# Performance work log

Hardware: AMD Instinct MI355X
Metric: run time of the kernel (lower is better)

The kernel has to match this reference:

```python
import jax, jax.numpy as jnp
import numpy as np

B, C, H, W = 16, 64, 64, 64
K = 512  # n_embeddings


def setup_inputs() -> dict:
    key = jax.random.key(0)
    k1, k2 = jax.random.split(key)
    inputs = jax.random.normal(k1, (B, C, H, W), dtype=jnp.float32)
    emb_weight = jax.random.normal(k2, (K, C), dtype=jnp.float32)
    weight = jnp.ones((K,), dtype=jnp.float32)  # EMA cluster-size buffer
    return {"inputs": inputs, "emb_weight": emb_weight, "weight": weight}


def reference(inputs, emb_weight, weight):
    sg = jax.lax.stop_gradient
    # BCHW -> BHWC
    x = jnp.transpose(inputs, (0, 2, 3, 1))  # [B,H,W,C]
    flat = x.reshape(-1, x.shape[-1])        # [N,C]
    n = flat.shape[0]
    k = emb_weight.shape[0]
    # squared euclidean distances [N,K] (argmin identical to cdist argmin)
    d = (
        jnp.sum(flat * flat, axis=-1, keepdims=True)
        - 2.0 * (flat @ emb_weight.T)
        + jnp.sum(emb_weight * emb_weight, axis=-1)
    )
    indices = jnp.argmin(d, axis=1)  # [N]
    # avg_probs = mean over rows of one-hot mask == normalized histogram
    avg_probs = jnp.bincount(indices, length=k).astype(jnp.float32) / jnp.float32(n)
    perplexity = jnp.exp(-jnp.sum(avg_probs * jnp.log(avg_probs + 1e-10)))
    # straight-through quantization
    q = emb_weight[indices].reshape(x.shape)  # [B,H,W,C]
    quantized = sg(q) + x - sg(x)
    commitment_loss = jnp.mean((sg(quantized) - x) ** 2)
    active_codes = jnp.sum(weight >= 0.01)
    out = jnp.transpose(quantized, (0, 3, 1, 2))  # back to BCHW
    return out, commitment_loss, perplexity, active_codes, indices
```

## Files before the change

kernel.cpp:

```cpp
#include <hip/hip_runtime.h>

#define HW 4096
#define CHW 262144
#define OUT_ELEMS 4194304
#define FLT_BIG 3.4e38f

typedef __attribute__((ext_vector_type(8))) short  short8;
typedef __attribute__((ext_vector_type(4))) float  floatx4;
typedef __attribute__((ext_vector_type(4))) int    intx4;


__device__ __forceinline__ unsigned bf16_rne(float f) {
    unsigned u = __float_as_uint(f);
    return (u + 0x7FFFu + ((u >> 16) & 1u)) >> 16;
}

__device__ __forceinline__ void split8(const float* f, intx4* hi, intx4* lo) {
    unsigned h[4], l[4];
#pragma unroll
    for (int j = 0; j < 4; ++j) {
        const unsigned h0 = bf16_rne(f[2 * j]);
        const unsigned h1 = bf16_rne(f[2 * j + 1]);
        const float hf0 = __uint_as_float(h0 << 16);
        const float hf1 = __uint_as_float(h1 << 16);
        const unsigned l0 = bf16_rne(f[2 * j] - hf0);
        const unsigned l1 = bf16_rne(f[2 * j + 1] - hf1);
        h[j] = h0 | (h1 << 16);
        l[j] = l0 | (l1 << 16);
    }
    *hi = intx4{(int)h[0], (int)h[1], (int)h[2], (int)h[3]};
    *lo = intx4{(int)l[0], (int)l[1], (int)l[2], (int)l[3]};
}

__global__ void vq_prep(const float* __restrict__ emb,
                        unsigned short* __restrict__ pfrag,
                        float* __restrict__ enorm) {
    const int t = threadIdx.x;
    const int lane = t & 63;
    const int code = (blockIdx.x << 2) + (t >> 6);
    const int c = lane;
    const float v = emb[(code << 6) + c];
    const unsigned hb = bf16_rne(v);
    const float hf    = __uint_as_float(hb << 16);
    const unsigned lb = bf16_rne(v - hf);
    const int nc = code >> 6, grp = (code & 63) >> 4, n = code & 15;
    const int q = (c & 31) >> 3, o = c & 7;
    const int jh = c >> 5;
    const int jl = 2 + (c >> 5);
    pfrag[((((size_t)(nc*4 + jh)*4 + grp)*4 + q)*16 + n)*8 + o] = (unsigned short)hb;
    pfrag[((((size_t)(nc*4 + jl)*4 + grp)*4 + q)*16 + n)*8 + o] = (unsigned short)lb;
    float s = v * v;
#pragma unroll
    for (int off = 32; off > 0; off >>= 1) s += __shfl_xor(s, off, 64);
    if (lane == 0) enorm[code] = -0.5f * s;
}

__global__ __launch_bounds__(256)
void vq_main(const float* __restrict__ x_in, const float* __restrict__ emb,
             const unsigned short* __restrict__ pfrag,
             const float* __restrict__ enorm,
             float* __restrict__ out, float* __restrict__ idx_out,
             double* __restrict__ ws_sse) {
    __shared__ float  b1s[2][32], b2s[2][32];
    __shared__ int    i1s[2][32], i2s[2][32];
    __shared__ int    c1i[32], c2i[32], qidx[32];
    __shared__ double parts[8][32];
    __shared__ double ls_red[4];

    const int t     = threadIdx.x;
    const int lane  = t & 63;
    const int wv    = t >> 6;
    const int col   = lane & 15;
    const int quad  = lane >> 4;
    const int blk   = blockIdx.x;
    const int mrow0 = (wv >> 1) << 4;
    const int khalf = wv & 1;
    const int ncol0 = khalf << 5;
    const int half = blk & 1;
    const int bh = blk >> 1;
    const int b = bh >> 6, h = bh & 63;
    const float* xb = x_in + (size_t)b * CHW + h * 64 + (half << 5);

    short8 Xh[2], Xl[2];
#pragma unroll
    for (int u = 0; u < 2; ++u) {
        float f[8];
#pragma unroll
        for (int j = 0; j < 8; ++j) {
            const int c = (u << 5) + (quad << 3) + j;
            f[j] = xb[(size_t)c * HW + mrow0 + col];
        }
        intx4 hi, lo;
        split8(f, &hi, &lo);
        Xh[u] = __builtin_bit_cast(short8, hi);
        Xl[u] = __builtin_bit_cast(short8, lo);
    }

    float B1a = -FLT_BIG, B2a = -FLT_BIG, B1b = -FLT_BIG, B2b = -FLT_BIG;
    int   I1a = 0x3FFFFFFF, I2a = 0x3FFFFFFF, I1b = 0x3FFFFFFF, I2b = 0x3FFFFFFF;

    const char*  pf  = (const char*)pfrag + (size_t)lane * 16 + ((size_t)khalf << 11);
    const float* enp = enorm + ncol0 + (quad << 2);

#pragma unroll 2
    for (int nc = 0; nc < 8; ++nc) {
        const char* base = pf + ((size_t)nc << 14);
        const int K0 = nc << 6;
        const floatx4 e0v = *(const floatx4*)(enp + K0);
        const floatx4 e1v = *(const floatx4*)(enp + K0 + 16);
        floatx4 a0{0.f,0.f,0.f,0.f}, a1{0.f,0.f,0.f,0.f};
#define BLD(j, g) (*(const short8*)(base + ((j) << 12) + ((g) << 10)))
        {
            const short8 e0 = BLD(0, 0), e1 = BLD(0, 1);
            a0 = __builtin_amdgcn_mfma_f32_16x16x32_bf16(e0, Xh[0], a0, 0, 0, 0);
            a1 = __builtin_amdgcn_mfma_f32_16x16x32_bf16(e1, Xh[0], a1, 0, 0, 0);
            a0 = __builtin_amdgcn_mfma_f32_16x16x32_bf16(e0, Xl[0], a0, 0, 0, 0);
            a1 = __builtin_amdgcn_mfma_f32_16x16x32_bf16(e1, Xl[0], a1, 0, 0, 0);
        }
        {
            const short8 e0 = BLD(1, 0), e1 = BLD(1, 1);
            a0 = __builtin_amdgcn_mfma_f32_16x16x32_bf16(e0, Xh[1], a0, 0, 0, 0);
            a1 = __builtin_amdgcn_mfma_f32_16x16x32_bf16(e1, Xh[1], a1, 0, 0, 0);
            a0 = __builtin_amdgcn_mfma_f32_16x16x32_bf16(e0, Xl[1], a0, 0, 0, 0);
            a1 = __builtin_amdgcn_mfma_f32_16x16x32_bf16(e1, Xl[1], a1, 0, 0, 0);
        }
        {
            const short8 e0 = BLD(2, 0), e1 = BLD(2, 1);
            a0 = __builtin_amdgcn_mfma_f32_16x16x32_bf16(e0, Xh[0], a0, 0, 0, 0);
            a1 = __builtin_amdgcn_mfma_f32_16x16x32_bf16(e1, Xh[0], a1, 0, 0, 0);
        }
        {
            const short8 e0 = BLD(3, 0), e1 = BLD(3, 1);
            a0 = __builtin_amdgcn_mfma_f32_16x16x32_bf16(e0, Xh[1], a0, 0, 0, 0);
            a1 = __builtin_amdgcn_mfma_f32_16x16x32_bf16(e1, Xh[1], a1, 0, 0, 0);
        }
#undef BLD

        const int cb = K0 + ncol0 + (quad << 2);
#pragma unroll
        for (int reg = 0; reg < 4; ++reg) {
            const float da = a0[reg] + e0v[reg];
            if (da > B1a)      { B2a = B1a; I2a = I1a; B1a = da; I1a = cb + reg; }
            else if (da > B2a) { B2a = da; I2a = cb + reg; }
            const float db = a1[reg] + e1v[reg];
            if (db > B1b)      { B2b = B1b; I2b = I1b; B1b = db; I1b = cb + 16 + reg; }
            else if (db > B2b) { B2b = db; I2b = cb + 16 + reg; }
        }
    }

    float B1, B2; int I1, I2;
    if (B1b > B1a || (B1b == B1a && I1b < I1a)) {
        B1 = B1b; I1 = I1b;
        if (B1a > B2b || (B1a == B2b && I1a < I2b)) { B2 = B1a; I2 = I1a; }
        else                                        { B2 = B2b; I2 = I2b; }
    } else {
        B1 = B1a; I1 = I1a;
        if (B1b > B2a || (B1b == B2a && I1b < I2a)) { B2 = B1b; I2 = I1b; }
        else                                        { B2 = B2a; I2 = I2a; }
    }

#pragma unroll
    for (int off = 16; off <= 32; off <<= 1) {
        const float ob1 = __shfl_xor(B1, off, 64);
        const int   oi1 = __shfl_xor(I1, off, 64);
        const float ob2 = __shfl_xor(B2, off, 64);
        const int   oi2 = __shfl_xor(I2, off, 64);
        if (ob1 > B1 || (ob1 == B1 && oi1 < I1)) {
            float nb2; int ni2;
            if (B1 > ob2 || (B1 == ob2 && I1 < oi2)) { nb2 = B1; ni2 = I1; }
            else                                     { nb2 = ob2; ni2 = oi2; }
            B1 = ob1; I1 = oi1; B2 = nb2; I2 = ni2;
        } else if (ob1 > B2 || (ob1 == B2 && oi1 < I2)) {
            B2 = ob1; I2 = oi1;
        }
    }
    if (lane < 16) {
        const int row = mrow0 + lane;
        b1s[khalf][row] = B1; b2s[khalf][row] = B2;
        i1s[khalf][row] = I1; i2s[khalf][row] = I2;
    }
    __syncthreads();

    if (t < 32) {
        const int r = t;
        float b1 = b1s[0][r], b2 = b2s[0][r];
        int   i1 = i1s[0][r], i2 = i2s[0][r];
        const float c1 = b1s[1][r]; const int j1 = i1s[1][r];
        const float c2 = b2s[1][r]; const int j2 = i2s[1][r];
        if (c1 > b1 || (c1 == b1 && j1 < i1))      { b2 = b1; i2 = i1; b1 = c1; i1 = j1; }
        else if (c1 > b2 || (c1 == b2 && j1 < i2)) { b2 = c1; i2 = j1; }
        if (c2 > b2 || (c2 == b2 && j2 < i2))      { b2 = c2; i2 = j2; }
        c1i[r] = i1; c2i[r] = i2;
    }
    __syncthreads();

    {
        const int r  = t & 31;
        const int k  = t >> 5;
        const int cq = k >> 1;
        const int code = (k & 1) ? c2i[r] : c1i[r];
        const float* ep = emb + ((size_t)code << 6) + (cq << 4);
        const float* xq = xb + r;
        double d0 = 0.0, d1 = 0.0;
#pragma unroll
        for (int cc = 0; cc < 16; cc += 2) {
            const int c = (cq << 4) + cc;
            const double f0 = (double)xq[(size_t)c * HW]       - (double)ep[cc];
            const double f1 = (double)xq[(size_t)(c + 1) * HW] - (double)ep[cc + 1];
            d0 = fma(f0, f0, d0);
            d1 = fma(f1, f1, d1);
        }
        parts[k][r] = d0 + d1;
    }
    __syncthreads();
    if (t < 32) {
        const double d1 = parts[0][t] + parts[2][t] + parts[4][t] + parts[6][t];
        const double d2 = parts[1][t] + parts[3][t] + parts[5][t] + parts[7][t];
        int i1 = c1i[t];
        const int i2 = c2i[t];
        if (d2 < d1 || (d2 == d1 && i2 < i1)) i1 = i2;
        qidx[t] = i1;
        idx_out[(blk << 5) + t] = (float)i1;
    }
    __syncthreads();

    {
        const int r  = t & 31;
        const int c0 = (t >> 5) << 3;
        const float* xp = xb + r;
        float*       op = out + (size_t)b * CHW + h * 64 + (half << 5) + r;
        const float* eq = emb + ((size_t)qidx[r] << 6);
        float sse_local = 0.f;
#pragma unroll
        for (int cc = 0; cc < 8; ++cc) {
            const int c = c0 + cc;
            const float qc = eq[c];
            const float dx = qc - xp[(size_t)c * HW];
            sse_local = fmaf(dx, dx, sse_local);
            op[(size_t)c * HW] = qc;
        }
#pragma unroll
        for (int off = 32; off > 0; off >>= 1)
            sse_local += __shfl_down(sse_local, off, 64);
        if (lane == 0) ls_red[wv] = (double)sse_local;
        __syncthreads();
        if (t == 0)
            ws_sse[blk] = (ls_red[0] + ls_red[1]) + (ls_red[2] + ls_red[3]);
    }
}

__global__ void vq_hist(const float* __restrict__ idx_out,
                        unsigned* __restrict__ part) {
    __shared__ unsigned hs[512];
    const int t = threadIdx.x;
    hs[t] = 0u; hs[t + 256] = 0u;
    __syncthreads();
    const float4* ip = (const float4*)(idx_out + (blockIdx.x << 12));
#pragma unroll
    for (int i = 0; i < 4; ++i) {
        const float4 v = ip[(i << 8) + t];
        atomicAdd(&hs[(int)v.x], 1u);
        atomicAdd(&hs[(int)v.y], 1u);
        atomicAdd(&hs[(int)v.z], 1u);
        atomicAdd(&hs[(int)v.w], 1u);
    }
    __syncthreads();
    unsigned* pp = part + (blockIdx.x << 9);
    pp[t] = hs[t]; pp[t + 256] = hs[t + 256];
}

__global__ void vq_scal(const unsigned* __restrict__ part,
                        const double* __restrict__ ws_sse,
                        const float* __restrict__ weight,
                        float* __restrict__ scal) {
    __shared__ double redt[8], reds[8];
    __shared__ int    redi[8];
    const int k = threadIdx.x;
    const int lane = k & 63, wv = k >> 6;
    unsigned cnt = 0;
#pragma unroll
    for (int p = 0; p < 16; ++p) cnt += part[(p << 9) + k];
    const double pr = (double)cnt / 65536.0;
    double term = pr * log(pr + 1e-10);
    double ssep = 0.0;
#pragma unroll
    for (int j = 0; j < 4; ++j) ssep += ws_sse[k + (j << 9)];
    int act = (weight[k] >= 0.01f) ? 1 : 0;
#pragma unroll
    for (int off = 32; off > 0; off >>= 1) {
        term += __shfl_down(term, off, 64);
        ssep += __shfl_down(ssep, off, 64);
        act  += __shfl_down(act,  off, 64);
    }
    if (lane == 0) { redt[wv] = term; reds[wv] = ssep; redi[wv] = act; }
    __syncthreads();
    if (k == 0) {
        double s = 0.0, ss = 0.0; int a = 0;
#pragma unroll
        for (int i = 0; i < 8; ++i) { s += redt[i]; ss += reds[i]; a += redi[i]; }
        scal[0] = (float)(ss / 4194304.0);
        scal[1] = (float)exp(-s);
        scal[2] = (float)a;
    }
}

extern "C" void kernel_launch(void* const* d_in, const int* in_sizes, int n_in,
                              void* d_out, int out_size, void* d_ws, size_t ws_size,
                              hipStream_t stream) {
    const float* x      = (const float*)d_in[0];
    const float* emb    = (const float*)d_in[1];
    const float* weight = (const float*)d_in[2];

    float* out = (float*)d_out;
    float*          enorm  = (float*)d_ws;
    unsigned short* pfrag  = (unsigned short*)((char*)d_ws + 4096);
    double*         ws_sse = (double*)((char*)d_ws + 135168);
    unsigned*       part   = (unsigned*)((char*)d_ws + 151552);

    float* scal    = out + OUT_ELEMS;
    float* idx_out = out + OUT_ELEMS + 3;

    vq_prep<<<128, 256, 0, stream>>>(emb, pfrag, enorm);
    vq_main<<<2048, 256, 0, stream>>>(x, emb, pfrag, enorm, out, idx_out, ws_sse);
    vq_hist<<<16, 256, 0, stream>>>(idx_out, part);
    vq_scal<<<1, 512, 0, stream>>>(part, ws_sse, weight, scal);
}
```

Before: 108.6 us.

## Halve vq_main block size and fuse histogram with scalar reduction

Each vq_main block now covers 16 pixels with two waves instead of 32 pixels with four, so the grid doubles to 4096 blocks of 128 threads. The final argmin pick is computed redundantly in every thread, which drops the shared qidx array and one barrier. The two small tail kernels (histogram and scalar reduction) are merged into one single-block kernel, removing a launch and the partial-histogram buffer. In exchange, one block must now do the whole 65536-entry histogram serially, and each pixel row is split into more, smaller blocks with less reuse of the codebook fragments per block.

```diff
diff --git a/kernel.cpp b/kernel.cpp
--- a/kernel.cpp
+++ b/kernel.cpp
@@ -55,17 +55,17 @@
     if (lane == 0) enorm[code] = -0.5f * s;
 }
 
-__global__ __launch_bounds__(256)
+__global__ __launch_bounds__(128)
 void vq_main(const float* __restrict__ x_in, const float* __restrict__ emb,
              const unsigned short* __restrict__ pfrag,
              const float* __restrict__ enorm,
              float* __restrict__ out, float* __restrict__ idx_out,
              double* __restrict__ ws_sse) {
-    __shared__ float  b1s[2][32], b2s[2][32];
-    __shared__ int    i1s[2][32], i2s[2][32];
-    __shared__ int    c1i[32], c2i[32], qidx[32];
-    __shared__ double parts[8][32];
-    __shared__ double ls_red[4];
+    __shared__ float  b1s[2][16], b2s[2][16];
+    __shared__ int    i1s[2][16], i2s[2][16];
+    __shared__ int    c1i[16], c2i[16];
+    __shared__ double parts[8][17];
+    __shared__ double ls_red[2];
 
     const int t     = threadIdx.x;
     const int lane  = t & 63;
@@ -73,13 +73,12 @@
     const int col   = lane & 15;
     const int quad  = lane >> 4;
     const int blk   = blockIdx.x;
-    const int mrow0 = (wv >> 1) << 4;
-    const int khalf = wv & 1;
+    const int khalf = wv;
     const int ncol0 = khalf << 5;
-    const int half = blk & 1;
-    const int bh = blk >> 1;
+    const int wq  = blk & 3;
+    const int bh  = blk >> 2;
     const int b = bh >> 6, h = bh & 63;
-    const float* xb = x_in + (size_t)b * CHW + h * 64 + (half << 5);
+    const float* xb = x_in + (size_t)b * CHW + h * 64 + (wq << 4);
 
     short8 Xh[2], Xl[2];
 #pragma unroll
@@ -88,7 +87,7 @@
 #pragma unroll
         for (int j = 0; j < 8; ++j) {
             const int c = (u << 5) + (quad << 3) + j;
-            f[j] = xb[(size_t)c * HW + mrow0 + col];
+            f[j] = xb[(size_t)c * HW + col];
         }
         intx4 hi, lo;
         split8(f, &hi, &lo);
@@ -175,13 +174,12 @@
         }
     }
     if (lane < 16) {
-        const int row = mrow0 + lane;
-        b1s[khalf][row] = B1; b2s[khalf][row] = B2;
-        i1s[khalf][row] = I1; i2s[khalf][row] = I2;
-    }
-    __syncthreads();
-
-    if (t < 32) {
+        b1s[khalf][lane] = B1; b2s[khalf][lane] = B2;
+        i1s[khalf][lane] = I1; i2s[khalf][lane] = I2;
+    }
+    __syncthreads();
+
+    if (t < 16) {
         const int r = t;
         float b1 = b1s[0][r], b2 = b2s[0][r];
         int   i1 = i1s[0][r], i2 = i2s[0][r];
@@ -194,9 +192,9 @@
     }
     __syncthreads();
 
+    const int r = t & 15;
+    const int k = t >> 4;
     {
-        const int r  = t & 31;
-        const int k  = t >> 5;
         const int cq = k >> 1;
         const int code = (k & 1) ? c2i[r] : c1i[r];
         const float* ep = emb + ((size_t)code << 6) + (cq << 4);
@@ -213,23 +211,22 @@
         parts[k][r] = d0 + d1;
     }
     __syncthreads();
-    if (t < 32) {
-        const double d1 = parts[0][t] + parts[2][t] + parts[4][t] + parts[6][t];
-        const double d2 = parts[1][t] + parts[3][t] + parts[5][t] + parts[7][t];
-        int i1 = c1i[t];
-        const int i2 = c2i[t];
-        if (d2 < d1 || (d2 == d1 && i2 < i1)) i1 = i2;
-        qidx[t] = i1;
-        idx_out[(blk << 5) + t] = (float)i1;
-    }
-    __syncthreads();
-
+
+    int win;
     {
-        const int r  = t & 31;
-        const int c0 = (t >> 5) << 3;
+        const double d1 = parts[0][r] + parts[2][r] + parts[4][r] + parts[6][r];
+        const double d2 = parts[1][r] + parts[3][r] + parts[5][r] + parts[7][r];
+        win = c1i[r];
+        const int i2 = c2i[r];
+        if (d2 < d1 || (d2 == d1 && i2 < win)) win = i2;
+        if (t < 16) idx_out[(blk << 4) + r] = (float)win;
+    }
+
+    {
+        const int c0 = k << 3;
         const float* xp = xb + r;
-        float*       op = out + (size_t)b * CHW + h * 64 + (half << 5) + r;
-        const float* eq = emb + ((size_t)qidx[r] << 6);
+        float*       op = out + (size_t)b * CHW + h * 64 + (wq << 4) + r;
+        const float* eq = emb + ((size_t)win << 6);
         float sse_local = 0.f;
 #pragma unroll
         for (int cc = 0; cc < 8; ++cc) {
@@ -245,47 +242,38 @@
         if (lane == 0) ls_red[wv] = (double)sse_local;
         __syncthreads();
         if (t == 0)
-            ws_sse[blk] = (ls_red[0] + ls_red[1]) + (ls_red[2] + ls_red[3]);
-    }
-}
-
-__global__ void vq_hist(const float* __restrict__ idx_out,
-                        unsigned* __restrict__ part) {
+            ws_sse[blk] = ls_red[0] + ls_red[1];
+    }
+}
+
+__global__ void vq_tail(const float* __restrict__ idx_out,
+                        const double* __restrict__ ws_sse,
+                        const float* __restrict__ weight,
+                        float* __restrict__ scal) {
     __shared__ unsigned hs[512];
+    __shared__ double redt[8], reds[8];
+    __shared__ int    redi[8];
     const int t = threadIdx.x;
-    hs[t] = 0u; hs[t + 256] = 0u;
-    __syncthreads();
-    const float4* ip = (const float4*)(idx_out + (blockIdx.x << 12));
-#pragma unroll
-    for (int i = 0; i < 4; ++i) {
-        const float4 v = ip[(i << 8) + t];
+    const int lane = t & 63, wv = t >> 6;
+    hs[t] = 0u;
+    __syncthreads();
+    const float4* ip = (const float4*)idx_out;
+#pragma unroll
+    for (int i = 0; i < 32; ++i) {
+        const float4 v = ip[(i << 9) + t];
         atomicAdd(&hs[(int)v.x], 1u);
         atomicAdd(&hs[(int)v.y], 1u);
         atomicAdd(&hs[(int)v.z], 1u);
         atomicAdd(&hs[(int)v.w], 1u);
     }
     __syncthreads();
-    unsigned* pp = part + (blockIdx.x << 9);
-    pp[t] = hs[t]; pp[t + 256] = hs[t + 256];
-}
-
-__global__ void vq_scal(const unsigned* __restrict__ part,
-                        const double* __restrict__ ws_sse,
-                        const float* __restrict__ weight,
-                        float* __restrict__ scal) {
-    __shared__ double redt[8], reds[8];
-    __shared__ int    redi[8];
-    const int k = threadIdx.x;
-    const int lane = k & 63, wv = k >> 6;
-    unsigned cnt = 0;
-#pragma unroll
-    for (int p = 0; p < 16; ++p) cnt += part[(p << 9) + k];
+    const unsigned cnt = hs[t];
     const double pr = (double)cnt / 65536.0;
     double term = pr * log(pr + 1e-10);
     double ssep = 0.0;
 #pragma unroll
-    for (int j = 0; j < 4; ++j) ssep += ws_sse[k + (j << 9)];
-    int act = (weight[k] >= 0.01f) ? 1 : 0;
+    for (int j = 0; j < 8; ++j) ssep += ws_sse[t + (j << 9)];
+    int act = (weight[t] >= 0.01f) ? 1 : 0;
 #pragma unroll
     for (int off = 32; off > 0; off >>= 1) {
         term += __shfl_down(term, off, 64);
@@ -294,7 +282,7 @@
     }
     if (lane == 0) { redt[wv] = term; reds[wv] = ssep; redi[wv] = act; }
     __syncthreads();
-    if (k == 0) {
+    if (t == 0) {
         double s = 0.0, ss = 0.0; int a = 0;
 #pragma unroll
         for (int i = 0; i < 8; ++i) { s += redt[i]; ss += reds[i]; a += redi[i]; }
@@ -315,13 +303,11 @@
     float*          enorm  = (float*)d_ws;
     unsigned short* pfrag  = (unsigned short*)((char*)d_ws + 4096);
     double*         ws_sse = (double*)((char*)d_ws + 135168);
-    unsigned*       part   = (unsigned*)((char*)d_ws + 151552);
 
     float* scal    = out + OUT_ELEMS;
     float* idx_out = out + OUT_ELEMS + 3;
 
     vq_prep<<<128, 256, 0, stream>>>(emb, pfrag, enorm);
-    vq_main<<<2048, 256, 0, stream>>>(x, emb, pfrag, enorm, out, idx_out, ws_sse);
-    vq_hist<<<16, 256, 0, stream>>>(idx_out, part);
-    vq_scal<<<1, 512, 0, stream>>>(part, ws_sse, weight, scal);
-}
+    vq_main<<<4096, 128, 0, stream>>>(x, emb, pfrag, enorm, out, idx_out, ws_sse);
+    vq_tail<<<1, 512, 0, stream>>>(idx_out, ws_sse, weight, scal);
+}
```

New measurement: 122.5 us. 12.7% more time.

## Process 64 rows per block so each codebook fragment load feeds two MFMA tiles

Applied to the files above, without the earlier changes.

Each wave now handles two 16-row tiles of pixels instead of one, so every codebook fragment loaded from global memory is reused across two sets of MFMAs. Blocks cover a full 64-pixel image row, which halves the grid, halves the number of SSE partials, and merges the winner selection into the final write phase, removing one barrier. The cost is higher register pressure from doubled accumulators and X fragments, and fewer blocks available to hide latency.

```diff
diff --git a/kernel.cpp b/kernel.cpp
--- a/kernel.cpp
+++ b/kernel.cpp
@@ -61,10 +61,10 @@
              const float* __restrict__ enorm,
              float* __restrict__ out, float* __restrict__ idx_out,
              double* __restrict__ ws_sse) {
-    __shared__ float  b1s[2][32], b2s[2][32];
-    __shared__ int    i1s[2][32], i2s[2][32];
-    __shared__ int    c1i[32], c2i[32], qidx[32];
-    __shared__ double parts[8][32];
+    __shared__ float  b1s[2][64], b2s[2][64];
+    __shared__ int    i1s[2][64], i2s[2][64];
+    __shared__ int    c1i[64], c2i[64];
+    __shared__ double parts[4][65];
     __shared__ double ls_red[4];
 
     const int t     = threadIdx.x;
@@ -73,31 +73,38 @@
     const int col   = lane & 15;
     const int quad  = lane >> 4;
     const int blk   = blockIdx.x;
-    const int mrow0 = (wv >> 1) << 4;
     const int khalf = wv & 1;
+    const int mset  = wv >> 1;
     const int ncol0 = khalf << 5;
-    const int half = blk & 1;
-    const int bh = blk >> 1;
-    const int b = bh >> 6, h = bh & 63;
-    const float* xb = x_in + (size_t)b * CHW + h * 64 + (half << 5);
-
-    short8 Xh[2], Xl[2];
-#pragma unroll
-    for (int u = 0; u < 2; ++u) {
-        float f[8];
-#pragma unroll
-        for (int j = 0; j < 8; ++j) {
-            const int c = (u << 5) + (quad << 3) + j;
-            f[j] = xb[(size_t)c * HW + mrow0 + col];
-        }
-        intx4 hi, lo;
-        split8(f, &hi, &lo);
-        Xh[u] = __builtin_bit_cast(short8, hi);
-        Xl[u] = __builtin_bit_cast(short8, lo);
-    }
-
-    float B1a = -FLT_BIG, B2a = -FLT_BIG, B1b = -FLT_BIG, B2b = -FLT_BIG;
-    int   I1a = 0x3FFFFFFF, I2a = 0x3FFFFFFF, I1b = 0x3FFFFFFF, I2b = 0x3FFFFFFF;
+    const int b = blk >> 6, h = blk & 63;
+    const float* xb = x_in + (size_t)b * CHW + h * 64;
+
+    short8 Xh[2][2], Xl[2][2];
+#pragma unroll
+    for (int T = 0; T < 2; ++T) {
+        const int row = (mset << 5) + (T << 4) + col;
+#pragma unroll
+        for (int u = 0; u < 2; ++u) {
+            float f[8];
+#pragma unroll
+            for (int j = 0; j < 8; ++j) {
+                const int c = (u << 5) + (quad << 3) + j;
+                f[j] = xb[(size_t)c * HW + row];
+            }
+            intx4 hi, lo;
+            split8(f, &hi, &lo);
+            Xh[T][u] = __builtin_bit_cast(short8, hi);
+            Xl[T][u] = __builtin_bit_cast(short8, lo);
+        }
+    }
+
+    float B1a[2], B2a[2], B1b[2], B2b[2];
+    int   I1a[2], I2a[2], I1b[2], I2b[2];
+#pragma unroll
+    for (int T = 0; T < 2; ++T) {
+        B1a[T] = -FLT_BIG; B2a[T] = -FLT_BIG; B1b[T] = -FLT_BIG; B2b[T] = -FLT_BIG;
+        I1a[T] = 0x3FFFFFFF; I2a[T] = 0x3FFFFFFF; I1b[T] = 0x3FFFFFFF; I2b[T] = 0x3FFFFFFF;
+    }
 
     const char*  pf  = (const char*)pfrag + (size_t)lane * 16 + ((size_t)khalf << 11);
     const float* enp = enorm + ncol0 + (quad << 2);
@@ -108,80 +115,98 @@
         const int K0 = nc << 6;
         const floatx4 e0v = *(const floatx4*)(enp + K0);
         const floatx4 e1v = *(const floatx4*)(enp + K0 + 16);
-        floatx4 a0{0.f,0.f,0.f,0.f}, a1{0.f,0.f,0.f,0.f};
+        floatx4 a0[2] = {{0.f,0.f,0.f,0.f},{0.f,0.f,0.f,0.f}};
+        floatx4 a1[2] = {{0.f,0.f,0.f,0.f},{0.f,0.f,0.f,0.f}};
 #define BLD(j, g) (*(const short8*)(base + ((j) << 12) + ((g) << 10)))
         {
             const short8 e0 = BLD(0, 0), e1 = BLD(0, 1);
-            a0 = __builtin_amdgcn_mfma_f32_16x16x32_bf16(e0, Xh[0], a0, 0, 0, 0);
-            a1 = __builtin_amdgcn_mfma_f32_16x16x32_bf16(e1, Xh[0], a1, 0, 0, 0);
-            a0 = __builtin_amdgcn_mfma_f32_16x16x32_bf16(e0, Xl[0], a0, 0, 0, 0);
-            a1 = __builtin_amdgcn_mfma_f32_16x16x32_bf16(e1, Xl[0], a1, 0, 0, 0);
+#pragma unroll
+            for (int T = 0; T < 2; ++T) {
+                a0[T] = __builtin_amdgcn_mfma_f32_16x16x32_bf16(e0, Xh[T][0], a0[T], 0, 0, 0);
+                a1[T] = __builtin_amdgcn_mfma_f32_16x16x32_bf16(e1, Xh[T][0], a1[T], 0, 0, 0);
+                a0[T] = __builtin_amdgcn_mfma_f32_16x16x32_bf16(e0, Xl[T][0], a0[T], 0, 0, 0);
+                a1[T] = __builtin_amdgcn_mfma_f32_16x16x32_bf16(e1, Xl[T][0], a1[T], 0, 0, 0);
+            }
         }
         {
             const short8 e0 = BLD(1, 0), e1 = BLD(1, 1);
-            a0 = __builtin_amdgcn_mfma_f32_16x16x32_bf16(e0, Xh[1], a0, 0, 0, 0);
-            a1 = __builtin_amdgcn_mfma_f32_16x16x32_bf16(e1, Xh[1], a1, 0, 0, 0);
-            a0 = __builtin_amdgcn_mfma_f32_16x16x32_bf16(e0, Xl[1], a0, 0, 0, 0);
-            a1 = __builtin_amdgcn_mfma_f32_16x16x32_bf16(e1, Xl[1], a1, 0, 0, 0);
+#pragma unroll
+            for (int T = 0; T < 2; ++T) {
+                a0[T] = __builtin_amdgcn_mfma_f32_16x16x32_bf16(e0, Xh[T][1], a0[T], 0, 0, 0);
+                a1[T] = __builtin_amdgcn_mfma_f32_16x16x32_bf16(e1, Xh[T][1], a1[T], 0, 0, 0);
+                a0[T] = __builtin_amdgcn_mfma_f32_16x16x32_bf16(e0, Xl[T][1], a0[T], 0, 0, 0);
+                a1[T] = __builtin_amdgcn_mfma_f32_16x16x32_bf16(e1, Xl[T][1], a1[T], 0, 0, 0);
+            }
         }
         {
             const short8 e0 = BLD(2, 0), e1 = BLD(2, 1);
-            a0 = __builtin_amdgcn_mfma_f32_16x16x32_bf16(e0, Xh[0], a0, 0, 0, 0);
-            a1 = __builtin_amdgcn_mfma_f32_16x16x32_bf16(e1, Xh[0], a1, 0, 0, 0);
+#pragma unroll
+            for (int T = 0; T < 2; ++T) {
+                a0[T] = __builtin_amdgcn_mfma_f32_16x16x32_bf16(e0, Xh[T][0], a0[T], 0, 0, 0);
+                a1[T] = __builtin_amdgcn_mfma_f32_16x16x32_bf16(e1, Xh[T][0], a1[T], 0, 0, 0);
+            }
         }
         {
             const short8 e0 = BLD(3, 0), e1 = BLD(3, 1);
-            a0 = __builtin_amdgcn_mfma_f32_16x16x32_bf16(e0, Xh[1], a0, 0, 0, 0);
-            a1 = __builtin_amdgcn_mfma_f32_16x16x32_bf16(e1, Xh[1], a1, 0, 0, 0);
+#pragma unroll
+            for (int T = 0; T < 2; ++T) {
+                a0[T] = __builtin_amdgcn_mfma_f32_16x16x32_bf16(e0, Xh[T][1], a0[T], 0, 0, 0);
+                a1[T] = __builtin_amdgcn_mfma_f32_16x16x32_bf16(e1, Xh[T][1], a1[T], 0, 0, 0);
+            }
         }
 #undef BLD
 
         const int cb = K0 + ncol0 + (quad << 2);
 #pragma unroll
-        for (int reg = 0; reg < 4; ++reg) {
-            const float da = a0[reg] + e0v[reg];
-            if (da > B1a)      { B2a = B1a; I2a = I1a; B1a = da; I1a = cb + reg; }
-            else if (da > B2a) { B2a = da; I2a = cb + reg; }
-            const float db = a1[reg] + e1v[reg];
-            if (db > B1b)      { B2b = B1b; I2b = I1b; B1b = db; I1b = cb + 16 + reg; }
-            else if (db > B2b) { B2b = db; I2b = cb + 16 + reg; }
-        }
-    }
-
-    float B1, B2; int I1, I2;
-    if (B1b > B1a || (B1b == B1a && I1b < I1a)) {
-        B1 = B1b; I1 = I1b;
-        if (B1a > B2b || (B1a == B2b && I1a < I2b)) { B2 = B1a; I2 = I1a; }
-        else                                        { B2 = B2b; I2 = I2b; }
-    } else {
-        B1 = B1a; I1 = I1a;
-        if (B1b > B2a || (B1b == B2a && I1b < I2a)) { B2 = B1b; I2 = I1b; }
-        else                                        { B2 = B2a; I2 = I2a; }
-    }
-
-#pragma unroll
-    for (int off = 16; off <= 32; off <<= 1) {
-        const float ob1 = __shfl_xor(B1, off, 64);
-        const int   oi1 = __shfl_xor(I1, off, 64);
-        const float ob2 = __shfl_xor(B2, off, 64);
-        const int   oi2 = __shfl_xor(I2, off, 64);
-        if (ob1 > B1 || (ob1 == B1 && oi1 < I1)) {
-            float nb2; int ni2;
-            if (B1 > ob2 || (B1 == ob2 && I1 < oi2)) { nb2 = B1; ni2 = I1; }
-            else                                     { nb2 = ob2; ni2 = oi2; }
-            B1 = ob1; I1 = oi1; B2 = nb2; I2 = ni2;
-        } else if (ob1 > B2 || (ob1 == B2 && oi1 < I2)) {
-            B2 = ob1; I2 = oi1;
-        }
-    }
-    if (lane < 16) {
-        const int row = mrow0 + lane;
-        b1s[khalf][row] = B1; b2s[khalf][row] = B2;
-        i1s[khalf][row] = I1; i2s[khalf][row] = I2;
-    }
-    __syncthreads();
-
-    if (t < 32) {
+        for (int T = 0; T < 2; ++T) {
+#pragma unroll
+            for (int reg = 0; reg < 4; ++reg) {
+                const float da = a0[T][reg] + e0v[reg];
+                if (da > B1a[T])      { B2a[T] = B1a[T]; I2a[T] = I1a[T]; B1a[T] = da; I1a[T] = cb + reg; }
+                else if (da > B2a[T]) { B2a[T] = da; I2a[T] = cb + reg; }
+                const float db = a1[T][reg] + e1v[reg];
+                if (db > B1b[T])      { B2b[T] = B1b[T]; I2b[T] = I1b[T]; B1b[T] = db; I1b[T] = cb + 16 + reg; }
+                else if (db > B2b[T]) { B2b[T] = db; I2b[T] = cb + 16 + reg; }
+            }
+        }
+    }
+
+#pragma unroll
+    for (int T = 0; T < 2; ++T) {
+        float B1, B2; int I1, I2;
+        if (B1b[T] > B1a[T] || (B1b[T] == B1a[T] && I1b[T] < I1a[T])) {
+            B1 = B1b[T]; I1 = I1b[T];
+            if (B1a[T] > B2b[T] || (B1a[T] == B2b[T] && I1a[T] < I2b[T])) { B2 = B1a[T]; I2 = I1a[T]; }
+            else                                                          { B2 = B2b[T]; I2 = I2b[T]; }
+        } else {
+            B1 = B1a[T]; I1 = I1a[T];
+            if (B1b[T] > B2a[T] || (B1b[T] == B2a[T] && I1b[T] < I2a[T])) { B2 = B1b[T]; I2 = I1b[T]; }
+            else                                                          { B2 = B2a[T]; I2 = I2a[T]; }
+        }
+#pragma unroll
+        for (int off = 16; off <= 32; off <<= 1) {
+            const float ob1 = __shfl_xor(B1, off, 64);
+            const int   oi1 = __shfl_xor(I1, off, 64);
+            const float ob2 = __shfl_xor(B2, off, 64);
+            const int   oi2 = __shfl_xor(I2, off, 64);
+            if (ob1 > B1 || (ob1 == B1 && oi1 < I1)) {
+                float nb2; int ni2;
+                if (B1 > ob2 || (B1 == ob2 && I1 < oi2)) { nb2 = B1; ni2 = I1; }
+                else                                     { nb2 = ob2; ni2 = oi2; }
+                B1 = ob1; I1 = oi1; B2 = nb2; I2 = ni2;
+            } else if (ob1 > B2 || (ob1 == B2 && oi1 < I2)) {
+                B2 = ob1; I2 = oi1;
+            }
+        }
+        if (lane < 16) {
+            const int row = (mset << 5) + (T << 4) + lane;
+            b1s[khalf][row] = B1; b2s[khalf][row] = B2;
+            i1s[khalf][row] = I1; i2s[khalf][row] = I2;
+        }
+    }
+    __syncthreads();
+
+    if (t < 64) {
         const int r = t;
         float b1 = b1s[0][r], b2 = b2s[0][r];
         int   i1 = i1s[0][r], i2 = i2s[0][r];
@@ -194,17 +219,17 @@
     }
     __syncthreads();
 
+    const int r = t & 63;
+    const int k = t >> 6;
     {
-        const int r  = t & 31;
-        const int k  = t >> 5;
-        const int cq = k >> 1;
+        const int ch = k >> 1;
         const int code = (k & 1) ? c2i[r] : c1i[r];
-        const float* ep = emb + ((size_t)code << 6) + (cq << 4);
+        const float* ep = emb + ((size_t)code << 6) + (ch << 5);
         const float* xq = xb + r;
         double d0 = 0.0, d1 = 0.0;
 #pragma unroll
-        for (int cc = 0; cc < 16; cc += 2) {
-            const int c = (cq << 4) + cc;
+        for (int cc = 0; cc < 32; cc += 2) {
+            const int c = (ch << 5) + cc;
             const double f0 = (double)xq[(size_t)c * HW]       - (double)ep[cc];
             const double f1 = (double)xq[(size_t)(c + 1) * HW] - (double)ep[cc + 1];
             d0 = fma(f0, f0, d0);
@@ -213,26 +238,25 @@
         parts[k][r] = d0 + d1;
     }
     __syncthreads();
-    if (t < 32) {
-        const double d1 = parts[0][t] + parts[2][t] + parts[4][t] + parts[6][t];
-        const double d2 = parts[1][t] + parts[3][t] + parts[5][t] + parts[7][t];
-        int i1 = c1i[t];
-        const int i2 = c2i[t];
-        if (d2 < d1 || (d2 == d1 && i2 < i1)) i1 = i2;
-        qidx[t] = i1;
-        idx_out[(blk << 5) + t] = (float)i1;
-    }
-    __syncthreads();
-
+
+    int win;
     {
-        const int r  = t & 31;
-        const int c0 = (t >> 5) << 3;
+        const double d1 = parts[0][r] + parts[2][r];
+        const double d2 = parts[1][r] + parts[3][r];
+        win = c1i[r];
+        const int i2 = c2i[r];
+        if (d2 < d1 || (d2 == d1 && i2 < win)) win = i2;
+        if (t < 64) idx_out[(blk << 6) + r] = (float)win;
+    }
+
+    {
+        const int c0 = k << 4;
         const float* xp = xb + r;
-        float*       op = out + (size_t)b * CHW + h * 64 + (half << 5) + r;
-        const float* eq = emb + ((size_t)qidx[r] << 6);
+        float*       op = out + (size_t)b * CHW + h * 64 + r;
+        const float* eq = emb + ((size_t)win << 6);
         float sse_local = 0.f;
 #pragma unroll
-        for (int cc = 0; cc < 8; ++cc) {
+        for (int cc = 0; cc < 16; ++cc) {
             const int c = c0 + cc;
             const float qc = eq[c];
             const float dx = qc - xp[(size_t)c * HW];
@@ -284,7 +308,7 @@
     double term = pr * log(pr + 1e-10);
     double ssep = 0.0;
 #pragma unroll
-    for (int j = 0; j < 4; ++j) ssep += ws_sse[k + (j << 9)];
+    for (int j = 0; j < 2; ++j) ssep += ws_sse[k + (j << 9)];
     int act = (weight[k] >= 0.01f) ? 1 : 0;
 #pragma unroll
     for (int off = 32; off > 0; off >>= 1) {
@@ -321,7 +345,7 @@
     float* idx_out = out + OUT_ELEMS + 3;
 
     vq_prep<<<128, 256, 0, stream>>>(emb, pfrag, enorm);
-    vq_main<<<2048, 256, 0, stream>>>(x, emb, pfrag, enorm, out, idx_out, ws_sse);
+    vq_main<<<1024, 256, 0, stream>>>(x, emb, pfrag, enorm, out, idx_out, ws_sse);
     vq_hist<<<16, 256, 0, stream>>>(idx_out, part);
     vq_scal<<<1, 512, 0, stream>>>(part, ws_sse, weight, scal);
 }
```

New measurement: 104.9 us. -3.5%, faster.
